# Kernel optimization log

Hardware: AMD Instinct MI355X
Metric: run time of the kernel (lower is better)

The kernel has to match this reference:

```python
import jax, jax.numpy as jnp
import numpy as np

D = 1024

def setup_inputs() -> dict:
    key = jax.random.key(0)
    k1, k2, k3, k4 = jax.random.split(key, 4)
    context = jax.random.normal(k1, (32, 2048, D), dtype=jnp.float32)
    # nn.Linear(dim, dim, bias=False): weight [D, D], applied as x @ W.T
    W = jax.random.normal(k2, (D, D), dtype=jnp.float32) / np.sqrt(D)
    # nn.Linear(dim, 1): weight [1, D], bias [1]
    v = jax.random.normal(k3, (D,), dtype=jnp.float32) / np.sqrt(D)
    b = jax.random.normal(k4, (), dtype=jnp.float32) * 0.01
    return {"context": context, "W": W, "v": v, "b": b}

def reference(context, W, v, b):
    # context: [B, S, D]
    h = jnp.tanh(jnp.einsum('bsd,ed->bse', context, W))      # [B, S, D]
    attn_logits = jnp.einsum('bsd,d->bs', h, v) + b          # [B, S]
    attn = jax.nn.softmax(attn_logits, axis=-1)              # softmax over sourceL
    weighted_context = jnp.einsum('bs,bsd->bd', attn, context)
    return weighted_context, attn
```

## Files before the change

kernel.cpp:

```cpp
#include <hip/hip_runtime.h>
#include <stdint.h>

#define BDIM 32
#define SDIM 2048
#define DDIM 1024
#define MDIM (BDIM * SDIM)

typedef __bf16 bf16x8 __attribute__((ext_vector_type(8)));
typedef float  f32x4  __attribute__((ext_vector_type(4)));


__device__ inline unsigned short f2bf(float f) {
  union { float f; unsigned u; } un; un.f = f;
  unsigned r = un.u + 0x7fffu + ((un.u >> 16) & 1u);
  return (unsigned short)(r >> 16);
}

__device__ inline float fast_tanh(float x) {
  float e = __expf(2.0f * x);
  return 1.0f - 2.0f / (e + 1.0f);
}

__device__ inline void gl_lds16(const unsigned short* g, unsigned short* l) {
  __builtin_amdgcn_global_load_lds(
      (__attribute__((address_space(1))) unsigned int*)(void*)(uintptr_t)g,
      (__attribute__((address_space(3))) unsigned int*)l,
      16, 0, 0);
}


__global__ __launch_bounds__(256) void cvt_kernel(const float* __restrict__ src,
                                                  unsigned short* __restrict__ dst) {
  size_t i = (size_t)blockIdx.x * 256 + threadIdx.x;
  const float4* s4 = (const float4*)src;
  float4 a = s4[2 * i];
  float4 b = s4[2 * i + 1];
  uint4 o;
  o.x = (unsigned)f2bf(a.x) | ((unsigned)f2bf(a.y) << 16);
  o.y = (unsigned)f2bf(a.z) | ((unsigned)f2bf(a.w) << 16);
  o.z = (unsigned)f2bf(b.x) | ((unsigned)f2bf(b.y) << 16);
  o.w = (unsigned)f2bf(b.z) | ((unsigned)f2bf(b.w) << 16);
  ((uint4*)dst)[i] = o;
}


__global__ __launch_bounds__(256) void gemm_logits(
    const float* __restrict__ ctx,
    const unsigned short* __restrict__ Bw,
    const float* __restrict__ v,
    float* __restrict__ logitsP)
{
  __shared__ __align__(16) unsigned short Al[128 * 64];
  __shared__ __align__(16) unsigned short Wl[128 * 64];

  const int t  = threadIdx.x;
  const int l  = (blockIdx.x & 7) * 512 + (blockIdx.x >> 3);
  const int mt = l >> 3;
  const int nt = l & 7;
  const int m0 = mt * 128;
  const int n0 = nt * 128;
  const int w    = t >> 6;
  const int lane = t & 63;
  const int c = lane & 15;
  const int q = lane >> 4;
  const int wm = (w >> 1) * 64;
  const int wn = (w & 1) * 64;

  float vv[4];
#pragma unroll
  for (int ni = 0; ni < 4; ++ni) vv[ni] = v[n0 + wn + ni * 16 + c];

  f32x4 acc[4][4] = {};

  const int rt  = t >> 3;
  const int sA  = t & 7;
  const int psl = sA ^ (rt & 7);
  const float* gA = ctx + (size_t)(m0 + rt) * DDIM + sA * 8;
  const unsigned short* gb = Bw + (size_t)(n0 + rt) * DDIM + psl * 8;
  unsigned short* lwb = Wl + (size_t)(t & 192) * 8;

  for (int kt = 0; kt < 16; ++kt) {
    const int k0 = kt * 64;
#pragma unroll
    for (int r = 0; r < 4; ++r)
      gl_lds16(gb + (size_t)(r * 32) * DDIM + k0, lwb + r * 2048);
#pragma unroll
    for (int j = 0; j < 4; ++j) {
      const int row = j * 32 + rt;
      const float* g = gA + (size_t)(j * 32) * DDIM + k0;
      float4 a = *(const float4*)g;
      float4 b = *(const float4*)(g + 4);
      bf16x8 cv;
      cv[0] = (__bf16)a.x; cv[1] = (__bf16)a.y;
      cv[2] = (__bf16)a.z; cv[3] = (__bf16)a.w;
      cv[4] = (__bf16)b.x; cv[5] = (__bf16)b.y;
      cv[6] = (__bf16)b.z; cv[7] = (__bf16)b.w;
      *(bf16x8*)&Al[row * 64 + psl * 8] = cv;
    }
    __syncthreads();

#pragma unroll
    for (int kk = 0; kk < 2; ++kk) {
      bf16x8 af[4], bfr[4];
      const int slot = ((kk * 4 + q) ^ (c & 7)) * 8;
#pragma unroll
      for (int mi = 0; mi < 4; ++mi)
        af[mi] = *(const bf16x8*)&Al[(wm + mi * 16 + c) * 64 + slot];
#pragma unroll
      for (int ni = 0; ni < 4; ++ni)
        bfr[ni] = *(const bf16x8*)&Wl[(wn + ni * 16 + c) * 64 + slot];
#pragma unroll
      for (int mi = 0; mi < 4; ++mi)
#pragma unroll
        for (int ni = 0; ni < 4; ++ni)
          acc[mi][ni] = __builtin_amdgcn_mfma_f32_16x16x32_bf16(
              af[mi], bfr[ni], acc[mi][ni], 0, 0, 0);
    }
    __syncthreads();
  }

  const size_t plane = (size_t)(nt * 2 + (w & 1)) * MDIM;
#pragma unroll
  for (int mi = 0; mi < 4; ++mi) {
    float p0 = 0.f, p1 = 0.f, p2 = 0.f, p3 = 0.f;
#pragma unroll
    for (int ni = 0; ni < 4; ++ni) {
      const float vvn = vv[ni];
      p0 += fast_tanh(acc[mi][ni][0]) * vvn;
      p1 += fast_tanh(acc[mi][ni][1]) * vvn;
      p2 += fast_tanh(acc[mi][ni][2]) * vvn;
      p3 += fast_tanh(acc[mi][ni][3]) * vvn;
    }
#pragma unroll
    for (int mask = 1; mask <= 8; mask <<= 1) {
      p0 += __shfl_xor(p0, mask);
      p1 += __shfl_xor(p1, mask);
      p2 += __shfl_xor(p2, mask);
      p3 += __shfl_xor(p3, mask);
    }
    if (c == 0) {
      float4 o = {p0, p1, p2, p3};
      *(float4*)(logitsP + plane + m0 + wm + mi * 16 + q * 4) = o;
    }
  }
}


__global__ __launch_bounds__(256) void softmax_kernel(const float* __restrict__ P,
                                                      float* __restrict__ attn) {
  const int b = blockIdx.x;
  const int t = threadIdx.x;
  float x[8];
#pragma unroll
  for (int i = 0; i < 8; ++i) {
    const size_t off = (size_t)b * SDIM + i * 256 + t;
    float s = 0.f;
#pragma unroll
    for (int pl = 0; pl < 16; ++pl) s += P[(size_t)pl * MDIM + off];
    x[i] = s;
  }
  float m = x[0];
#pragma unroll
  for (int i = 1; i < 8; ++i) m = fmaxf(m, x[i]);
#pragma unroll
  for (int mask = 1; mask < 64; mask <<= 1) m = fmaxf(m, __shfl_xor(m, mask));
  __shared__ float redm[4], reds[4];
  const int w = t >> 6, lane = t & 63;
  if (lane == 0) redm[w] = m;
  __syncthreads();
  m = fmaxf(fmaxf(redm[0], redm[1]), fmaxf(redm[2], redm[3]));
  float e[8];
  float s = 0.f;
#pragma unroll
  for (int i = 0; i < 8; ++i) { e[i] = __expf(x[i] - m); s += e[i]; }
#pragma unroll
  for (int mask = 1; mask < 64; mask <<= 1) s += __shfl_xor(s, mask);
  if (lane == 0) reds[w] = s;
  __syncthreads();
  s = reds[0] + reds[1] + reds[2] + reds[3];
  const float inv = 1.0f / s;
  float* p = attn + (size_t)b * SDIM;
#pragma unroll
  for (int i = 0; i < 8; ++i) p[i * 256 + t] = e[i] * inv;
}


__global__ __launch_bounds__(256) void wsum_part(const float* __restrict__ ctx,
                                                 const float* __restrict__ attn,
                                                 float* __restrict__ part) {
  const int b  = blockIdx.x >> 6;
  const int sc = blockIdx.x & 63;
  const int t  = threadIdx.x;
  const float* cp = ctx + ((size_t)b * SDIM + sc * 32) * DDIM + t * 4;
  const float* ap = attn + (size_t)b * SDIM + sc * 32;
  float4 acc = {0.f, 0.f, 0.f, 0.f};
#pragma unroll 4
  for (int s = 0; s < 32; ++s) {
    const float a = ap[s];
    const float4 cv = *(const float4*)(cp + (size_t)s * DDIM);
    acc.x += a * cv.x; acc.y += a * cv.y; acc.z += a * cv.z; acc.w += a * cv.w;
  }
  *(float4*)(part + (size_t)blockIdx.x * DDIM + t * 4) = acc;
}


__global__ __launch_bounds__(256) void wsum_reduce(const float* __restrict__ part,
                                                   float* __restrict__ wc) {
  const int b = blockIdx.x >> 2;
  const int d = (blockIdx.x & 3) * 256 + threadIdx.x;
  float s = 0.f;
#pragma unroll
  for (int sc = 0; sc < 64; ++sc)
    s += part[((size_t)b * 64 + sc) * DDIM + d];
  wc[(size_t)b * DDIM + d] = s;
}


extern "C" void kernel_launch(void* const* d_in, const int* in_sizes, int n_in,
                              void* d_out, int out_size, void* d_ws, size_t ws_size,
                              hipStream_t stream) {
  const float* ctx = (const float*)d_in[0];
  const float* W   = (const float*)d_in[1];
  const float* v   = (const float*)d_in[2];

  float* out_wc   = (float*)d_out;
  float* out_attn = out_wc + BDIM * DDIM;

  float* logitsP = (float*)d_ws;
  float* part    = logitsP + (size_t)16 * MDIM;
  unsigned short* W_bf = (unsigned short*)(part + (size_t)2048 * DDIM);

  cvt_kernel<<<(DDIM * DDIM) / (256 * 8), 256, 0, stream>>>(W, W_bf);
  gemm_logits<<<(MDIM / 128) * (DDIM / 128), 256, 0, stream>>>(ctx, W_bf, v, logitsP);
  softmax_kernel<<<BDIM, 256, 0, stream>>>(logitsP, out_attn);
  wsum_part<<<BDIM * 64, 256, 0, stream>>>(ctx, out_attn, part);
  wsum_reduce<<<(BDIM * DDIM) / 256, 256, 0, stream>>>(part, out_wc);
}
```

Baseline: 557.0 us.

## Double-buffer GEMM LDS tiles with register prefetch of fp32 context

The logits GEMM now keeps two LDS buffers for both the A (context) and W tiles. The next W tile is loaded asynchronously while the current tile feeds the MFMAs, and the context tile is prefetched into registers two steps ahead, then converted and written to LDS after compute. This leaves one barrier per k-step instead of two and raises wave priority around the MFMA block, aiming to hide global-load latency behind matrix math. The cost is double the LDS footprint and extra prefetch registers, which may lower occupancy.

Result: slower. 583.3 us (+4.7%).

```diff
diff --git a/kernel.cpp b/kernel.cpp
--- a/kernel.cpp
+++ b/kernel.cpp
@@ -5,6 +5,7 @@
 #define SDIM 2048
 #define DDIM 1024
 #define MDIM (BDIM * SDIM)
+#define K_STEPS 16
 
 typedef __bf16 bf16x8 __attribute__((ext_vector_type(8)));
 typedef float  f32x4  __attribute__((ext_vector_type(4)));
@@ -50,8 +51,8 @@
     const float* __restrict__ v,
     float* __restrict__ logitsP)
 {
-  __shared__ __align__(16) unsigned short Al[128 * 64];
-  __shared__ __align__(16) unsigned short Wl[128 * 64];
+  __shared__ __align__(16) unsigned short Al[2][128 * 64];
+  __shared__ __align__(16) unsigned short Wl[2][128 * 64];
 
   const int t  = threadIdx.x;
   const int l  = (blockIdx.x & 7) * 512 + (blockIdx.x >> 3);
@@ -77,38 +78,62 @@
   const int psl = sA ^ (rt & 7);
   const float* gA = ctx + (size_t)(m0 + rt) * DDIM + sA * 8;
   const unsigned short* gb = Bw + (size_t)(n0 + rt) * DDIM + psl * 8;
-  unsigned short* lwb = Wl + (size_t)(t & 192) * 8;
-
-  for (int kt = 0; kt < 16; ++kt) {
-    const int k0 = kt * 64;
-#pragma unroll
-    for (int r = 0; r < 4; ++r)
-      gl_lds16(gb + (size_t)(r * 32) * DDIM + k0, lwb + r * 2048);
+  const int lwoff = (t & 192) * 8;
+
+  float4 pa[4][2];
+
+  auto A_LOAD = [&](int kt) {
+#pragma unroll
+    for (int j = 0; j < 4; ++j) {
+      const float* g = gA + (size_t)(j * 32) * DDIM + kt * 64;
+      pa[j][0] = *(const float4*)g;
+      pa[j][1] = *(const float4*)(g + 4);
+    }
+  };
+  auto A_WRITE = [&](int buf) {
 #pragma unroll
     for (int j = 0; j < 4; ++j) {
       const int row = j * 32 + rt;
-      const float* g = gA + (size_t)(j * 32) * DDIM + k0;
-      float4 a = *(const float4*)g;
-      float4 b = *(const float4*)(g + 4);
       bf16x8 cv;
-      cv[0] = (__bf16)a.x; cv[1] = (__bf16)a.y;
-      cv[2] = (__bf16)a.z; cv[3] = (__bf16)a.w;
-      cv[4] = (__bf16)b.x; cv[5] = (__bf16)b.y;
-      cv[6] = (__bf16)b.z; cv[7] = (__bf16)b.w;
-      *(bf16x8*)&Al[row * 64 + psl * 8] = cv;
-    }
-    __syncthreads();
-
+      cv[0] = (__bf16)pa[j][0].x; cv[1] = (__bf16)pa[j][0].y;
+      cv[2] = (__bf16)pa[j][0].z; cv[3] = (__bf16)pa[j][0].w;
+      cv[4] = (__bf16)pa[j][1].x; cv[5] = (__bf16)pa[j][1].y;
+      cv[6] = (__bf16)pa[j][1].z; cv[7] = (__bf16)pa[j][1].w;
+      *(bf16x8*)&Al[buf][row * 64 + psl * 8] = cv;
+    }
+  };
+  auto W_ISSUE = [&](int kt, int buf) {
+#pragma unroll
+    for (int r = 0; r < 4; ++r)
+      gl_lds16(gb + (size_t)(r * 32) * DDIM + kt * 64,
+               &Wl[buf][r * 2048 + lwoff]);
+  };
+
+  A_LOAD(0);
+  W_ISSUE(0, 0);
+  asm volatile("s_waitcnt vmcnt(0)" ::: "memory");
+  A_WRITE(0);
+  A_LOAD(1);
+  asm volatile("s_waitcnt lgkmcnt(0)" ::: "memory");
+  __builtin_amdgcn_s_barrier();
+
+#pragma unroll 2
+  for (int kt = 0; kt < K_STEPS; ++kt) {
+    const int cur = kt & 1;
+    const int nxt = cur ^ 1;
+    if (kt + 1 < K_STEPS) W_ISSUE(kt + 1, nxt);
+
+    __builtin_amdgcn_s_setprio(1);
 #pragma unroll
     for (int kk = 0; kk < 2; ++kk) {
       bf16x8 af[4], bfr[4];
       const int slot = ((kk * 4 + q) ^ (c & 7)) * 8;
 #pragma unroll
       for (int mi = 0; mi < 4; ++mi)
-        af[mi] = *(const bf16x8*)&Al[(wm + mi * 16 + c) * 64 + slot];
+        af[mi] = *(const bf16x8*)&Al[cur][(wm + mi * 16 + c) * 64 + slot];
 #pragma unroll
       for (int ni = 0; ni < 4; ++ni)
-        bfr[ni] = *(const bf16x8*)&Wl[(wn + ni * 16 + c) * 64 + slot];
+        bfr[ni] = *(const bf16x8*)&Wl[cur][(wn + ni * 16 + c) * 64 + slot];
 #pragma unroll
       for (int mi = 0; mi < 4; ++mi)
 #pragma unroll
@@ -116,7 +141,15 @@
           acc[mi][ni] = __builtin_amdgcn_mfma_f32_16x16x32_bf16(
               af[mi], bfr[ni], acc[mi][ni], 0, 0, 0);
     }
-    __syncthreads();
+    __builtin_amdgcn_s_setprio(0);
+
+    if (kt + 1 < K_STEPS) {
+      asm volatile("s_waitcnt vmcnt(0)" ::: "memory");
+      A_WRITE(nxt);
+      if (kt + 2 < K_STEPS) A_LOAD(kt + 2);
+    }
+    asm volatile("s_waitcnt lgkmcnt(0)" ::: "memory");
+    __builtin_amdgcn_s_barrier();
   }
 
   const size_t plane = (size_t)(nt * 2 + (w & 1)) * MDIM;
```
